# Optimization experiments

Measured on AMD Instinct MI355X. Metric: run time of the kernel, lower is better.

The kernel has to match this reference:

```python
import jax, jax.numpy as jnp
import numpy as np

N_EMBD = 768
N_HEAD = 12
HEAD_DIM = N_EMBD // N_HEAD


def setup_inputs() -> dict:
    key = jax.random.key(0)
    ks = jax.random.split(key, 5)
    B, T, C = 1, 4096, N_EMBD
    s = 1.0 / np.sqrt(C)
    return {
        "x": jax.random.normal(ks[0], (B, T, C), dtype=jnp.float32),
        "wq": jax.random.normal(ks[1], (C, C), dtype=jnp.float32) * s,
        "wk": jax.random.normal(ks[2], (C, C), dtype=jnp.float32) * s,
        "wv": jax.random.normal(ks[3], (C, C), dtype=jnp.float32) * s,
        "wo": jax.random.normal(ks[4], (C, C), dtype=jnp.float32) * s,
    }


def reference(x, wq, wk, wv, wo):
    B, T, C = x.shape
    H, D = N_HEAD, HEAD_DIM
    # projections: torch Linear(y = x @ W^T); weights stored as (out, in)
    q = (x @ wq.T).reshape(B, T, H, D).transpose(0, 2, 1, 3)  # B H T D
    k = (x @ wk.T).reshape(B, T, H, D).transpose(0, 2, 1, 3)
    v = (x @ wv.T).reshape(B, T, H, D).transpose(0, 2, 1, 3)
    scale = 1.0 / jnp.sqrt(jnp.asarray(D, dtype=x.dtype))
    attn = jnp.einsum("bhtd,bhsd->bhts", q, k) * scale  # B H T T
    causal = jnp.tril(jnp.ones((T, T), dtype=bool))
    attn = jnp.where(causal, attn, -jnp.inf)
    attn = jax.nn.softmax(attn, axis=-1)
    out = jnp.einsum("bhts,bhsd->bhtd", attn, v)  # B H T D
    out = out.transpose(0, 2, 1, 3).reshape(B, T, C)
    return out @ wo.T
```

## Files before the change

kernel.cpp:

```cpp
#include <hip/hip_runtime.h>


#define T_SEQ 4096
#define C_EMB 768
#define NH    12
#define HD    64

typedef __attribute__((ext_vector_type(8))) short bf16x8;
typedef __attribute__((ext_vector_type(4))) float floatx4;

#define QSCALE 0.18033688011112042f

__device__ __forceinline__ unsigned short f2bf(float f) {
  union { float f; unsigned u; } v; v.f = f;
  unsigned r = v.u + 0x7fffu + ((v.u >> 16) & 1u);
  return (unsigned short)(r >> 16);
}
__device__ __forceinline__ unsigned short f2bf_rhu(float f) {
  union { float f; unsigned u; } v; v.f = f;
  return (unsigned short)((v.u + 0x8000u) >> 16);
}
__device__ __forceinline__ float bf2f(unsigned short h) {
  union { unsigned u; float f; } v; v.u = ((unsigned)h) << 16;
  return v.f;
}

__device__ __forceinline__ void gload_lds16(const void* gptr, void* ldsptr) {
  __builtin_amdgcn_global_load_lds(
      (const __attribute__((address_space(1))) unsigned int*)gptr,
      (__attribute__((address_space(3))) unsigned int*)ldsptr,
      16, 0, 0);
}

__global__ void cast_all_kernel(const float* __restrict__ x,
                                const float* __restrict__ wq,
                                const float* __restrict__ wk,
                                const float* __restrict__ wv,
                                const float* __restrict__ wo,
                                unsigned short* __restrict__ dst) {
  const int GX = (T_SEQ * C_EMB) / 4;
  const int GW = (C_EMB * C_EMB) / 4;
  int i = blockIdx.x * blockDim.x + threadIdx.x;
  const float* src; int local;
  if (i < GX) { src = x; local = i; }
  else {
    int t = i - GX; int w = t / GW; local = t - w * GW;
    src = (w == 0) ? wq : (w == 1) ? wk : (w == 2) ? wv : wo;
  }
  float4 f = reinterpret_cast<const float4*>(src)[local];
  ushort4 u;
  u.x = f2bf(f.x); u.y = f2bf(f.y); u.z = f2bf(f.z); u.w = f2bf(f.w);
  reinterpret_cast<ushort4*>(dst)[i] = u;
}

__global__ __launch_bounds__(256) void gemm_qkv(
    const unsigned short* __restrict__ A,
    const unsigned short* __restrict__ B,
    unsigned short* __restrict__ Qb,
    unsigned short* __restrict__ Kb,
    unsigned short* __restrict__ Vt) {
  constexpr int K = 768, BM = 64, BN = 128, BK = 64;
  __shared__ __align__(16) unsigned short As0[BM * BK];
  __shared__ __align__(16) unsigned short Bs0[BN * BK];
  __shared__ __align__(16) unsigned short As1[BM * BK];
  __shared__ __align__(16) unsigned short Bs1[BN * BK];
  const int tid = threadIdx.x;
  const int wave = tid >> 6, lane = tid & 63;
  const int lm = lane & 15, lq = lane >> 4;
  const int swz = lm & 7;
  const int m0 = blockIdx.x * BM, n0 = blockIdx.y * BN;
  const int wm = (wave & 1) * 32, wn = (wave >> 1) * 64;
  floatx4 acc[2][4] = {};

  auto stage = [&](int k0, unsigned short* Ad, unsigned short* Bd) {
#pragma unroll
    for (int i = 0; i < 2; i++) {
      int idx = i * 256 + tid;
      int row = idx >> 3;
      int ch = (idx & 7) ^ (row & 7);
      gload_lds16(A + (size_t)(m0 + row) * K + k0 + ch * 8, (char*)Ad + idx * 16);
    }
#pragma unroll
    for (int i = 0; i < 4; i++) {
      int idx = i * 256 + tid;
      int row = idx >> 3;
      int ch = (idx & 7) ^ (row & 7);
      gload_lds16(B + (size_t)(n0 + row) * K + k0 + ch * 8, (char*)Bd + idx * 16);
    }
  };

  auto compute = [&](const unsigned short* Asb, const unsigned short* Bsb) {
#pragma unroll
    for (int kk = 0; kk < 2; kk++) {
      bf16x8 af[2], bfr[4];
#pragma unroll
      for (int i = 0; i < 2; i++) {
        int row = wm + i * 16 + lm;
        af[i] = *(const bf16x8*)(Asb + row * BK + (((kk * 4 + lq) ^ swz) * 8));
      }
#pragma unroll
      for (int j = 0; j < 4; j++) {
        int row = wn + j * 16 + lm;
        bfr[j] = *(const bf16x8*)(Bsb + row * BK + (((kk * 4 + lq) ^ swz) * 8));
      }
#pragma unroll
      for (int i = 0; i < 2; i++)
#pragma unroll
        for (int j = 0; j < 4; j++)
          acc[i][j] = __builtin_amdgcn_mfma_f32_16x16x32_bf16(af[i], bfr[j], acc[i][j], 0, 0, 0);
    }
  };

  stage(0, As0, Bs0);
  int k0 = 0;
  while (true) {
    __syncthreads();
    if (k0 + BK < K) stage(k0 + BK, As1, Bs1);
    compute(As0, Bs0);
    k0 += BK; if (k0 >= K) break;
    __syncthreads();
    if (k0 + BK < K) stage(k0 + BK, As0, Bs0);
    compute(As1, Bs1);
    k0 += BK; if (k0 >= K) break;
  }

  const int which = n0 / C_EMB;
  if (which < 2) {
    unsigned short* tgt = (which == 0) ? Qb : Kb;
    const float sc = (which == 0) ? QSCALE : 1.0f;
#pragma unroll
    for (int i = 0; i < 2; i++)
#pragma unroll
      for (int j = 0; j < 4; j++) {
        int n = n0 - which * C_EMB + wn + j * 16 + lm;
        int h = n >> 6, d = n & 63;
#pragma unroll
        for (int r = 0; r < 4; r++) {
          int m = m0 + wm + i * 16 + lq * 4 + r;
          tgt[(((size_t)h * T_SEQ + m) << 6) + d] = f2bf(acc[i][j][r] * sc);
        }
      }
  } else {
#pragma unroll
    for (int i = 0; i < 2; i++)
#pragma unroll
      for (int j = 0; j < 4; j++) {
        int n = n0 - 2 * C_EMB + wn + j * 16 + lm;
        int h = n >> 6, d = n & 63;
        int m = m0 + wm + i * 16 + lq * 4;
        ushort4 pk;
        pk.x = f2bf(acc[i][j][0]); pk.y = f2bf(acc[i][j][1]);
        pk.z = f2bf(acc[i][j][2]); pk.w = f2bf(acc[i][j][3]);
        *(ushort4*)(Vt + ((size_t)(h * HD + d)) * T_SEQ + m) = pk;
      }
  }
}

struct AttnState {
  float rsum[2];
  floatx4 o_acc[2][4];
};

template <typename EpilogueFn>
__device__ __forceinline__ void attn_body(
    const unsigned short* __restrict__ Q,
    const unsigned short* __restrict__ K,
    const unsigned short* __restrict__ Vt,
    int h, int q0, int sb, int se,
    EpilogueFn epi) {
  constexpr int BS = 64, PS = 72, KVB = BS * HD;
  __shared__ __align__(16) unsigned short Ks0[KVB];
  __shared__ __align__(16) unsigned short Vs0[KVB];
  __shared__ __align__(16) unsigned short Ks1[KVB];
  __shared__ __align__(16) unsigned short Vs1[KVB];
  __shared__ __align__(16) unsigned short Ps[4 * 32 * PS];

  const int tid = threadIdx.x;
  const int wave = tid >> 6, lane = tid & 63;
  const int lm = lane & 15, lq = lane >> 4;
  const unsigned short* Qh = Q + (size_t)h * T_SEQ * HD;
  const unsigned short* Kh = K + (size_t)h * T_SEQ * HD;
  const unsigned short* Vh = Vt + (size_t)h * HD * T_SEQ;
  const int qrow_base = q0 + wave * 32;
  unsigned short* Pw = Ps + wave * 32 * PS;
  const int swz = lm & 7;

  bf16x8 qf[2][2];
#pragma unroll
  for (int m = 0; m < 2; m++)
#pragma unroll
    for (int kk = 0; kk < 2; kk++)
      qf[m][kk] = *(const bf16x8*)(Qh + (size_t)(qrow_base + m * 16 + lm) * HD + kk * 32 + lq * 8);

  AttnState st;
#pragma unroll
  for (int m = 0; m < 2; m++) {
    st.rsum[m] = 0.f;
#pragma unroll
    for (int r = 0; r < 4; r++) st.o_acc[m][r] = floatx4{0.f, 0.f, 0.f, 0.f};
  }

  auto stage = [&](int s0, unsigned short* Kd, unsigned short* Vd) {
#pragma unroll
    for (int i = 0; i < 2; i++) {
      int idx = (wave * 2 + i) * 64 + lane;
      int row = idx >> 3;
      int ch = (idx & 7) ^ (row & 7);
      gload_lds16(Kh + (size_t)(s0 + row) * HD + ch * 8, (char*)Kd + idx * 16);
      gload_lds16(Vh + (size_t)row * T_SEQ + s0 + ch * 8, (char*)Vd + idx * 16);
    }
  };

  auto compute = [&](int it, const unsigned short* Kc, const unsigned short* Vc) {
    const int s0 = it * BS;
    floatx4 sa[2][4] = {};
#pragma unroll
    for (int kk = 0; kk < 2; kk++)
#pragma unroll
      for (int j = 0; j < 4; j++) {
        int row = j * 16 + lm;
        bf16x8 kf = *(const bf16x8*)(Kc + (row * 8 + ((kk * 4 + lq) ^ swz)) * 8);
#pragma unroll
        for (int m = 0; m < 2; m++)
          sa[m][j] = __builtin_amdgcn_mfma_f32_16x16x32_bf16(kf, qf[m][kk], sa[m][j], 0, 0, 0);
      }

    if (s0 >= q0) {
#pragma unroll
      for (int m = 0; m < 2; m++) {
        int qrow = qrow_base + m * 16 + lm;
#pragma unroll
        for (int j = 0; j < 4; j++)
#pragma unroll
          for (int r = 0; r < 4; r++) {
            int scol = s0 + j * 16 + lq * 4 + r;
            if (scol > qrow) sa[m][j][r] = -1e30f;
          }
      }
    }

#pragma unroll
    for (int m = 0; m < 2; m++)
#pragma unroll
      for (int j = 0; j < 4; j++) {
        float p0 = __builtin_amdgcn_exp2f(sa[m][j][0]);
        float p1 = __builtin_amdgcn_exp2f(sa[m][j][1]);
        float p2 = __builtin_amdgcn_exp2f(sa[m][j][2]);
        float p3 = __builtin_amdgcn_exp2f(sa[m][j][3]);
        st.rsum[m] += (p0 + p1) + (p2 + p3);
        ushort4 pk;
        pk.x = f2bf_rhu(p0); pk.y = f2bf_rhu(p1);
        pk.z = f2bf_rhu(p2); pk.w = f2bf_rhu(p3);
        *(ushort4*)(Pw + (m * 16 + lm) * PS + j * 16 + lq * 4) = pk;
      }

#pragma unroll
    for (int kk = 0; kk < 2; kk++) {
      bf16x8 pf[2];
#pragma unroll
      for (int m = 0; m < 2; m++)
        pf[m] = *(const bf16x8*)(Pw + (m * 16 + lm) * PS + kk * 32 + lq * 8);
#pragma unroll
      for (int jd = 0; jd < 4; jd++) {
        int row = jd * 16 + lm;
        bf16x8 vf = *(const bf16x8*)(Vc + (row * 8 + ((kk * 4 + lq) ^ swz)) * 8);
#pragma unroll
        for (int m = 0; m < 2; m++)
          st.o_acc[m][jd] = __builtin_amdgcn_mfma_f32_16x16x32_bf16(pf[m], vf, st.o_acc[m][jd], 0, 0, 0);
      }
    }
  };

  stage(sb * BS, Ks0, Vs0);
  int it = sb;
  while (true) {
    __syncthreads();
    if (it + 1 < se) stage((it + 1) * BS, Ks1, Vs1);
    compute(it, Ks0, Vs0);
    if (++it >= se) break;
    __syncthreads();
    if (it + 1 < se) stage((it + 1) * BS, Ks0, Vs0);
    compute(it, Ks1, Vs1);
    if (++it >= se) break;
  }

#pragma unroll
  for (int m = 0; m < 2; m++) {
    float s = st.rsum[m];
    s += __shfl_xor(s, 16);
    s += __shfl_xor(s, 32);
    st.rsum[m] = s;
  }
  epi(st, qrow_base, lm, lq);
}

__global__ __launch_bounds__(256, 3) void attn_kernelA(
    const unsigned short* __restrict__ Q,
    const unsigned short* __restrict__ K,
    const unsigned short* __restrict__ Vt,
    float* __restrict__ Opart,
    float* __restrict__ lpart) {
  const int bid = blockIdx.x;
  const int h = bid % NH;
  const int z = bid / NH;
  const int qt = (T_SEQ / 128 - 1) - (z >> 1);
  const int c = z & 1;
  const int q0 = qt * 128;
  const int sb = c ? (qt + 1) : 0;
  const int se = c ? (2 * qt + 2) : (qt + 1);

  const size_t CN = (size_t)NH * T_SEQ * HD;
  float* Oc = Opart + (size_t)c * CN;
  float* lc = lpart + (size_t)c * NH * T_SEQ;
  attn_body(Q, K, Vt, h, q0, sb, se,
    [&](const AttnState& st, int qrow_base, int lm, int lq) {
#pragma unroll
      for (int m = 0; m < 2; m++) {
        if (lq == 0) lc[h * T_SEQ + qrow_base + m * 16 + lm] = st.rsum[m];
#pragma unroll
        for (int r = 0; r < 4; r++) {
          int t = qrow_base + m * 16 + lq * 4 + r;
#pragma unroll
          for (int jd = 0; jd < 4; jd++)
            Oc[((size_t)h * T_SEQ + t) * HD + jd * 16 + lm] = st.o_acc[m][jd][r];
        }
      }
    });
}

__global__ void combine_kernelA(const float* __restrict__ Opart,
                                const float* __restrict__ lpart,
                                unsigned short* __restrict__ Ob) {
  int idx = blockIdx.x * blockDim.x + threadIdx.x;
  int d4 = idx & 15;
  int t = (idx >> 4) & (T_SEQ - 1);
  int h = idx >> 16;
  const size_t CN4 = (size_t)NH * T_SEQ * HD / 4;
  float4 a = reinterpret_cast<const float4*>(Opart)[idx];
  float4 b = reinterpret_cast<const float4*>(Opart)[CN4 + idx];
  float l = lpart[h * T_SEQ + t] + lpart[NH * T_SEQ + h * T_SEQ + t];
  float inv = 1.0f / l;
  ushort4 u;
  u.x = f2bf((a.x + b.x) * inv); u.y = f2bf((a.y + b.y) * inv);
  u.z = f2bf((a.z + b.z) * inv); u.w = f2bf((a.w + b.w) * inv);
  *(ushort4*)(Ob + (size_t)t * C_EMB + h * HD + d4 * 4) = u;
}

__global__ __launch_bounds__(256, 3) void attn_kernel2(
    const unsigned short* __restrict__ Q,
    const unsigned short* __restrict__ K,
    const unsigned short* __restrict__ Vt,
    unsigned short* __restrict__ Op0,
    unsigned short* __restrict__ Op1,
    float* __restrict__ lpart) {
  const int bid = blockIdx.x;
  const int h = bid % NH;
  const int z = bid / NH;
  const int qt = (T_SEQ / 128 - 1) - (z >> 1);
  const int c = z & 1;
  const int q0 = qt * 128;
  const int sb = c ? (qt + 1) : 0;
  const int se = c ? (2 * qt + 2) : (qt + 1);

  unsigned short* Oc = c ? Op1 : Op0;
  float* lc = lpart + (size_t)c * NH * T_SEQ;
  attn_body(Q, K, Vt, h, q0, sb, se,
    [&](const AttnState& st, int qrow_base, int lm, int lq) {
#pragma unroll
      for (int m = 0; m < 2; m++) {
        if (lq == 0) lc[h * T_SEQ + qrow_base + m * 16 + lm] = st.rsum[m];
#pragma unroll
        for (int r = 0; r < 4; r++) {
          int t = qrow_base + m * 16 + lq * 4 + r;
#pragma unroll
          for (int jd = 0; jd < 4; jd++)
            Oc[((size_t)h * T_SEQ + t) * HD + jd * 16 + lm] = f2bf(st.o_acc[m][jd][r]);
        }
      }
    });
}

__global__ void combine_kernel2(const unsigned short* __restrict__ Op0,
                                const unsigned short* __restrict__ Op1,
                                const float* __restrict__ lpart,
                                unsigned short* __restrict__ Ob) {
  int idx = blockIdx.x * blockDim.x + threadIdx.x;
  int d4 = idx & 15;
  int t = (idx >> 4) & (T_SEQ - 1);
  int h = idx >> 16;
  float l = lpart[h * T_SEQ + t] + lpart[NH * T_SEQ + h * T_SEQ + t];
  float inv = 1.0f / l;
  ushort4 a = reinterpret_cast<const ushort4*>(Op0)[idx];
  ushort4 b = reinterpret_cast<const ushort4*>(Op1)[idx];
  ushort4 u;
  u.x = f2bf((bf2f(a.x) + bf2f(b.x)) * inv);
  u.y = f2bf((bf2f(a.y) + bf2f(b.y)) * inv);
  u.z = f2bf((bf2f(a.z) + bf2f(b.z)) * inv);
  u.w = f2bf((bf2f(a.w) + bf2f(b.w)) * inv);
  *(ushort4*)(Ob + (size_t)t * C_EMB + h * HD + d4 * 4) = u;
}

__global__ __launch_bounds__(256) void gemm_out(
    const unsigned short* __restrict__ A,
    const unsigned short* __restrict__ B,
    float* __restrict__ Out) {
  constexpr int K = 768, BM = 64, BN = 128, BK = 64;
  __shared__ __align__(16) unsigned short As0[BM * BK];
  __shared__ __align__(16) unsigned short Bs0[BN * BK];
  __shared__ __align__(16) unsigned short As1[BM * BK];
  __shared__ __align__(16) unsigned short Bs1[BN * BK];
  const int tid = threadIdx.x;
  const int wave = tid >> 6, lane = tid & 63;
  const int lm = lane & 15, lq = lane >> 4;
  const int swz = lm & 7;
  const int m0 = blockIdx.x * BM, n0 = blockIdx.y * BN;
  const int wm = (wave & 1) * 32, wn = (wave >> 1) * 64;
  floatx4 acc[2][4] = {};

  auto stage = [&](int k0, unsigned short* Ad, unsigned short* Bd) {
#pragma unroll
    for (int i = 0; i < 2; i++) {
      int idx = i * 256 + tid;
      int row = idx >> 3;
      int ch = (idx & 7) ^ (row & 7);
      gload_lds16(A + (size_t)(m0 + row) * K + k0 + ch * 8, (char*)Ad + idx * 16);
    }
#pragma unroll
    for (int i = 0; i < 4; i++) {
      int idx = i * 256 + tid;
      int row = idx >> 3;
      int ch = (idx & 7) ^ (row & 7);
      gload_lds16(B + (size_t)(n0 + row) * K + k0 + ch * 8, (char*)Bd + idx * 16);
    }
  };

  auto compute = [&](const unsigned short* Asb, const unsigned short* Bsb) {
#pragma unroll
    for (int kk = 0; kk < 2; kk++) {
      bf16x8 af[2], bfr[4];
#pragma unroll
      for (int i = 0; i < 2; i++) {
        int row = wm + i * 16 + lm;
        af[i] = *(const bf16x8*)(Asb + row * BK + (((kk * 4 + lq) ^ swz) * 8));
      }
#pragma unroll
      for (int j = 0; j < 4; j++) {
        int row = wn + j * 16 + lm;
        bfr[j] = *(const bf16x8*)(Bsb + row * BK + (((kk * 4 + lq) ^ swz) * 8));
      }
#pragma unroll
      for (int i = 0; i < 2; i++)
#pragma unroll
        for (int j = 0; j < 4; j++)
          acc[i][j] = __builtin_amdgcn_mfma_f32_16x16x32_bf16(af[i], bfr[j], acc[i][j], 0, 0, 0);
    }
  };

  stage(0, As0, Bs0);
  int k0 = 0;
  while (true) {
    __syncthreads();
    if (k0 + BK < K) stage(k0 + BK, As1, Bs1);
    compute(As0, Bs0);
    k0 += BK; if (k0 >= K) break;
    __syncthreads();
    if (k0 + BK < K) stage(k0 + BK, As0, Bs0);
    compute(As1, Bs1);
    k0 += BK; if (k0 >= K) break;
  }

#pragma unroll
  for (int i = 0; i < 2; i++)
#pragma unroll
    for (int j = 0; j < 4; j++)
#pragma unroll
      for (int r = 0; r < 4; r++) {
        int m = m0 + wm + i * 16 + lq * 4 + r;
        int n = n0 + wn + j * 16 + lm;
        Out[(size_t)m * C_EMB + n] = acc[i][j][r];
      }
}

extern "C" void kernel_launch(void* const* d_in, const int* in_sizes, int n_in,
                              void* d_out, int out_size, void* d_ws, size_t ws_size,
                              hipStream_t stream) {
  const float* x  = (const float*)d_in[0];
  const float* wq = (const float*)d_in[1];
  const float* wk = (const float*)d_in[2];
  const float* wv = (const float*)d_in[3];
  const float* wo = (const float*)d_in[4];
  float* out = (float*)d_out;

  const size_t XN = (size_t)T_SEQ * C_EMB;
  const size_t WN = (size_t)C_EMB * C_EMB;
  unsigned short* base = (unsigned short*)d_ws;

  unsigned short* Xb   = base;
  unsigned short* Wqkv = base + XN;
  unsigned short* Wob  = base + XN + 3 * WN;
  unsigned short* Qb   = base + XN + 4 * WN;
  unsigned short* Kb   = Qb + XN;
  unsigned short* Vt   = Kb + XN;
  unsigned short* tail = Vt + XN;
  unsigned short* Ob   = Qb;

  const size_t needA = 29884416ull + 2ull * XN * 4ull + 2ull * NH * T_SEQ * 4ull;

  const int ngroups = (int)((XN + 4 * WN) / 4);
  cast_all_kernel<<<dim3(ngroups / 256), 256, 0, stream>>>(x, wq, wk, wv, wo, Xb);

  gemm_qkv<<<dim3(T_SEQ / 64, 2304 / 128), 256, 0, stream>>>(Xb, Wqkv, Qb, Kb, Vt);

  if (ws_size >= needA) {
    float* OpartA = (float*)tail;
    float* lpartA = OpartA + 2 * XN;
    attn_kernelA<<<dim3((T_SEQ / 128) * 2 * NH), 256, 0, stream>>>(Qb, Kb, Vt, OpartA, lpartA);
    combine_kernelA<<<dim3((int)(XN / 4) / 256), 256, 0, stream>>>(OpartA, lpartA, Ob);
  } else {
    unsigned short* Op0 = base;
    unsigned short* Op1 = tail;
    float* lpart = (float*)(base + XN);
    attn_kernel2<<<dim3((T_SEQ / 128) * 2 * NH), 256, 0, stream>>>(Qb, Kb, Vt, Op0, Op1, lpart);
    combine_kernel2<<<dim3((int)(XN / 4) / 256), 256, 0, stream>>>(Op0, Op1, lpart, Ob);
  }

  gemm_out<<<dim3(T_SEQ / 64, C_EMB / 128), 256, 0, stream>>>(Ob, Wob, out);
}
```

Before: 156.1 us.

## Software-pipeline attention so PV MFMAs of previous block overlap next QK

Restructures the attention inner loop so the P·V matrix multiply for block i is issued in the same phase as the QK^T multiply for block i+1. P and V fragments are loaded into registers at the end of each phase and consumed in the next, with a prologue phase and a final drain of the last P·V. The aim is to hide the exp/convert/LDS round-trip latency behind independent MFMA work. In exchange, 12 extra bf16x8 registers stay live across iterations, which may raise register pressure and affect the occupancy target of 3 blocks.

New measurement: 261.7 us. 67.6% more time.

```diff
diff --git a/kernel.cpp b/kernel.cpp
--- a/kernel.cpp
+++ b/kernel.cpp
@@ -161,6 +161,70 @@
   floatx4 o_acc[2][4];
 };
 
+#define ATTN_PHASE(Kc, Vc, DO_PV, S0V)                                        \
+  {                                                                           \
+    const int s0_ = (S0V);                                                    \
+    floatx4 sa[2][4] = {};                                                    \
+    _Pragma("unroll")                                                         \
+    for (int kk = 0; kk < 2; kk++)                                            \
+      _Pragma("unroll")                                                       \
+      for (int j = 0; j < 4; j++) {                                           \
+        int row_ = j * 16 + lm;                                               \
+        bf16x8 kf = *(const bf16x8*)((Kc) + (row_ * 8 + ((kk * 4 + lq) ^ swz)) * 8); \
+        _Pragma("unroll")                                                     \
+        for (int m = 0; m < 2; m++)                                           \
+          sa[m][j] = __builtin_amdgcn_mfma_f32_16x16x32_bf16(kf, qf[m][kk], sa[m][j], 0, 0, 0); \
+      }                                                                       \
+    if (DO_PV) {                                                              \
+      _Pragma("unroll")                                                       \
+      for (int kk = 0; kk < 2; kk++)                                          \
+        _Pragma("unroll")                                                     \
+        for (int jd = 0; jd < 4; jd++)                                        \
+          _Pragma("unroll")                                                   \
+          for (int m = 0; m < 2; m++)                                         \
+            st.o_acc[m][jd] = __builtin_amdgcn_mfma_f32_16x16x32_bf16(pfp[m][kk], vfp[kk][jd], st.o_acc[m][jd], 0, 0, 0); \
+    }                                                                         \
+    if (s0_ >= q0) {                                                          \
+      _Pragma("unroll")                                                       \
+      for (int m = 0; m < 2; m++) {                                           \
+        int qrow_ = qrow_base + m * 16 + lm;                                  \
+        _Pragma("unroll")                                                     \
+        for (int j = 0; j < 4; j++)                                           \
+          _Pragma("unroll")                                                   \
+          for (int r = 0; r < 4; r++) {                                       \
+            int scol_ = s0_ + j * 16 + lq * 4 + r;                            \
+            if (scol_ > qrow_) sa[m][j][r] = -1e30f;                          \
+          }                                                                   \
+      }                                                                       \
+    }                                                                         \
+    _Pragma("unroll")                                                         \
+    for (int m = 0; m < 2; m++)                                               \
+      _Pragma("unroll")                                                       \
+      for (int j = 0; j < 4; j++) {                                           \
+        float p0 = __builtin_amdgcn_exp2f(sa[m][j][0]);                       \
+        float p1 = __builtin_amdgcn_exp2f(sa[m][j][1]);                       \
+        float p2 = __builtin_amdgcn_exp2f(sa[m][j][2]);                       \
+        float p3 = __builtin_amdgcn_exp2f(sa[m][j][3]);                       \
+        st.rsum[m] += (p0 + p1) + (p2 + p3);                                  \
+        ushort4 pk;                                                           \
+        pk.x = f2bf_rhu(p0); pk.y = f2bf_rhu(p1);                             \
+        pk.z = f2bf_rhu(p2); pk.w = f2bf_rhu(p3);                             \
+        *(ushort4*)(Pw + (m * 16 + lm) * PS + j * 16 + lq * 4) = pk;          \
+      }                                                                       \
+    _Pragma("unroll")                                                         \
+    for (int kk = 0; kk < 2; kk++)                                            \
+      _Pragma("unroll")                                                       \
+      for (int m = 0; m < 2; m++)                                             \
+        pfp[m][kk] = *(const bf16x8*)(Pw + (m * 16 + lm) * PS + kk * 32 + lq * 8); \
+    _Pragma("unroll")                                                         \
+    for (int kk = 0; kk < 2; kk++)                                            \
+      _Pragma("unroll")                                                       \
+      for (int jd = 0; jd < 4; jd++) {                                        \
+        int row_ = jd * 16 + lm;                                              \
+        vfp[kk][jd] = *(const bf16x8*)((Vc) + (row_ * 8 + ((kk * 4 + lq) ^ swz)) * 8); \
+      }                                                                       \
+  }
+
 template <typename EpilogueFn>
 __device__ __forceinline__ void attn_body(
     const unsigned short* __restrict__ Q,
@@ -200,6 +264,9 @@
     for (int r = 0; r < 4; r++) st.o_acc[m][r] = floatx4{0.f, 0.f, 0.f, 0.f};
   }
 
+  bf16x8 pfp[2][2] = {};
+  bf16x8 vfp[2][4] = {};
+
   auto stage = [&](int s0, unsigned short* Kd, unsigned short* Vd) {
 #pragma unroll
     for (int i = 0; i < 2; i++) {
@@ -211,78 +278,31 @@
     }
   };
 
-  auto compute = [&](int it, const unsigned short* Kc, const unsigned short* Vc) {
-    const int s0 = it * BS;
-    floatx4 sa[2][4] = {};
-#pragma unroll
-    for (int kk = 0; kk < 2; kk++)
-#pragma unroll
-      for (int j = 0; j < 4; j++) {
-        int row = j * 16 + lm;
-        bf16x8 kf = *(const bf16x8*)(Kc + (row * 8 + ((kk * 4 + lq) ^ swz)) * 8);
-#pragma unroll
-        for (int m = 0; m < 2; m++)
-          sa[m][j] = __builtin_amdgcn_mfma_f32_16x16x32_bf16(kf, qf[m][kk], sa[m][j], 0, 0, 0);
-      }
-
-    if (s0 >= q0) {
-#pragma unroll
-      for (int m = 0; m < 2; m++) {
-        int qrow = qrow_base + m * 16 + lm;
-#pragma unroll
-        for (int j = 0; j < 4; j++)
-#pragma unroll
-          for (int r = 0; r < 4; r++) {
-            int scol = s0 + j * 16 + lq * 4 + r;
-            if (scol > qrow) sa[m][j][r] = -1e30f;
-          }
-      }
-    }
-
-#pragma unroll
-    for (int m = 0; m < 2; m++)
-#pragma unroll
-      for (int j = 0; j < 4; j++) {
-        float p0 = __builtin_amdgcn_exp2f(sa[m][j][0]);
-        float p1 = __builtin_amdgcn_exp2f(sa[m][j][1]);
-        float p2 = __builtin_amdgcn_exp2f(sa[m][j][2]);
-        float p3 = __builtin_amdgcn_exp2f(sa[m][j][3]);
-        st.rsum[m] += (p0 + p1) + (p2 + p3);
-        ushort4 pk;
-        pk.x = f2bf_rhu(p0); pk.y = f2bf_rhu(p1);
-        pk.z = f2bf_rhu(p2); pk.w = f2bf_rhu(p3);
-        *(ushort4*)(Pw + (m * 16 + lm) * PS + j * 16 + lq * 4) = pk;
-      }
-
-#pragma unroll
-    for (int kk = 0; kk < 2; kk++) {
-      bf16x8 pf[2];
-#pragma unroll
-      for (int m = 0; m < 2; m++)
-        pf[m] = *(const bf16x8*)(Pw + (m * 16 + lm) * PS + kk * 32 + lq * 8);
-#pragma unroll
-      for (int jd = 0; jd < 4; jd++) {
-        int row = jd * 16 + lm;
-        bf16x8 vf = *(const bf16x8*)(Vc + (row * 8 + ((kk * 4 + lq) ^ swz)) * 8);
-#pragma unroll
-        for (int m = 0; m < 2; m++)
-          st.o_acc[m][jd] = __builtin_amdgcn_mfma_f32_16x16x32_bf16(pf[m], vf, st.o_acc[m][jd], 0, 0, 0);
-      }
-    }
-  };
-
   stage(sb * BS, Ks0, Vs0);
   int it = sb;
-  while (true) {
-    __syncthreads();
-    if (it + 1 < se) stage((it + 1) * BS, Ks1, Vs1);
-    compute(it, Ks0, Vs0);
-    if (++it >= se) break;
-    __syncthreads();
-    if (it + 1 < se) stage((it + 1) * BS, Ks0, Vs0);
-    compute(it, Ks1, Vs1);
-    if (++it >= se) break;
-  }
+  __syncthreads();
+  if (it + 1 < se) stage((it + 1) * BS, Ks1, Vs1);
+  ATTN_PHASE(Ks0, Vs0, false, it * BS);
+  ++it;
+  if (it < se) {
+    while (true) {
+      __syncthreads();
+      if (it + 1 < se) stage((it + 1) * BS, Ks0, Vs0);
+      ATTN_PHASE(Ks1, Vs1, true, it * BS);
+      if (++it >= se) break;
+      __syncthreads();
+      if (it + 1 < se) stage((it + 1) * BS, Ks1, Vs1);
+      ATTN_PHASE(Ks0, Vs0, true, it * BS);
+      if (++it >= se) break;
+    }
+  }
+#pragma unroll
+  for (int kk = 0; kk < 2; kk++)
+#pragma unroll
+    for (int jd = 0; jd < 4; jd++)
+#pragma unroll
+      for (int m = 0; m < 2; m++)
+        st.o_acc[m][jd] = __builtin_amdgcn_mfma_f32_16x16x32_bf16(pfp[m][kk], vfp[kk][jd], st.o_acc[m][jd], 0, 0, 0);
 
 #pragma unroll
   for (int m = 0; m < 2; m++) {
```
